# Performance work log

Hardware: AMD Instinct MI355X
Metric: run time of the kernel (lower is better)

The kernel has to match this reference:

```python
import jax, jax.numpy as jnp
import numpy as np

N = 100000
E = 3200000
IN_F = 256
OUT_F = 64
ALPHA = 0.2  # LeakyReLU negative slope


def setup_inputs() -> dict:
    key = jax.random.key(0)
    k1, k2, k3, k4 = jax.random.split(key, 4)
    adj = jax.random.randint(k1, (2, E), 0, N, dtype=jnp.int64)
    x = jax.random.normal(k2, (N, IN_F), dtype=jnp.float32)
    # xavier-normal-ish scales
    W_fc = jax.random.normal(k3, (OUT_F, IN_F), dtype=jnp.float32) * (1.414 * np.sqrt(2.0 / (IN_F + OUT_F)))
    b_fc = jnp.zeros((OUT_F,), dtype=jnp.float32)
    a = jax.random.normal(k4, (1, 2 * OUT_F), dtype=jnp.float32) * (1.414 * np.sqrt(2.0 / (1 + 2 * OUT_F)))
    return {"adj": adj, "x": x, "W_fc": W_fc, "b_fc": b_fc, "a": a}


def reference(adj, x, W_fc, b_fc, a):
    src = adj[0]  # [E]
    dst = adj[1]  # [E]
    h = x @ W_fc.T + b_fc                       # [N, OUT_F]
    a1, a2 = a[0, :OUT_F], a[0, OUT_F:]         # split of attention vector
    # e = leakyrelu(a . [h_src || h_dst]) computed without materializing concat
    s1 = h @ a1                                  # [N]
    s2 = h @ a2                                  # [N]
    e = s1[src] + s2[dst]                        # [E]
    e = jnp.where(e > 0, e, ALPHA * e)           # LeakyReLU
    # dgl edge_softmax: softmax over edges grouped by destination node
    m = jax.ops.segment_max(e, dst, num_segments=N)     # [N]
    ex = jnp.exp(e - m[dst])                             # [E]
    denom = jax.ops.segment_sum(ex, dst, num_segments=N) # [N]
    att = ex / denom[dst]                                # [E]
    # SparseTensor(row=src, col=dst, value=att) @ h -> out[src] += att * h[dst]
    h_prime = jax.ops.segment_sum(att[:, None] * h[dst], src, num_segments=N)  # [N, OUT_F]
    return jax.nn.elu(h_prime)  # concat=True branch
```

## Files before the change

kernel.cpp:

```cpp
#include <hip/hip_runtime.h>
#include <math.h>

#define N_NODES 100000
#define N_EDGES 3200000
#define IN_F 256
#define OUT_F 64
#define LRELU_ALPHA 0.2f
#define NBKT 782
#define CAP 4480

typedef unsigned short u16;
typedef __attribute__((ext_vector_type(8))) short short8;
typedef __attribute__((ext_vector_type(4))) float floatx4;

__device__ inline u16 f2bf(float f) {
  unsigned u = __float_as_uint(f);
  u += 0x7FFFu + ((u >> 16) & 1u);
  return (u16)(u >> 16);
}
__device__ inline float bf2f(u16 h) {
  return __uint_as_float(((unsigned)h) << 16);
}

__global__ __launch_bounds__(256) void k_prep(const float* __restrict__ W,
                                              u16* __restrict__ Wbf,
                                              int* __restrict__ sfill,
                                              int* __restrict__ dfill) {
  if (blockIdx.x < 64) {
    int i = blockIdx.x * 256 + threadIdx.x;
    Wbf[i] = f2bf(W[i]);
  } else {
    for (int i = threadIdx.x; i < NBKT; i += 256) {
      sfill[i] = 0;
      dfill[i] = 0;
    }
  }
}

__global__ __launch_bounds__(256) void k_linear(
    const float* __restrict__ x, const u16* __restrict__ Wbf,
    const float* __restrict__ b, const float* __restrict__ a,
    u16* __restrict__ hbf, float* __restrict__ s1, float* __restrict__ s2) {
  __shared__ u16 Wlds[64 * 264];

  const int t = threadIdx.x;
#pragma unroll
  for (int p = 0; p < 8; p++) {
    int c = p * 256 + t;
    int row = c >> 5;
    int kc = (c & 31) * 8;
    *(short8*)&Wlds[row * 264 + kc] = *(const short8*)&Wbf[row * 256 + kc];
  }
  __syncthreads();

  const int w = t >> 6;
  const int lane = t & 63;
  const int col = lane & 15;
  const int q = lane >> 4;
  const int m0 = blockIdx.x * 64 + w * 16;

  floatx4 acc[4];
#pragma unroll
  for (int nt = 0; nt < 4; nt++) acc[nt] = (floatx4){0.f, 0.f, 0.f, 0.f};

  int mrow = m0 + col;
  if (mrow > N_NODES - 1) mrow = N_NODES - 1;
  const float* xrow = x + (size_t)mrow * IN_F + q * 8;

#pragma unroll
  for (int kk = 0; kk < 8; kk++) {
    float4 f0 = *(const float4*)(xrow + kk * 32);
    float4 f1 = *(const float4*)(xrow + kk * 32 + 4);
    short8 af;
    af[0] = (short)f2bf(f0.x);
    af[1] = (short)f2bf(f0.y);
    af[2] = (short)f2bf(f0.z);
    af[3] = (short)f2bf(f0.w);
    af[4] = (short)f2bf(f1.x);
    af[5] = (short)f2bf(f1.y);
    af[6] = (short)f2bf(f1.z);
    af[7] = (short)f2bf(f1.w);
#pragma unroll
    for (int nt = 0; nt < 4; nt++) {
      short8 bfr = *(const short8*)&Wlds[(nt * 16 + col) * 264 + kk * 32 + q * 8];
      acc[nt] = __builtin_amdgcn_mfma_f32_16x16x32_bf16(af, bfr, acc[nt], 0, 0, 0);
    }
  }

  float bv[4], a1v[4], a2v[4];
#pragma unroll
  for (int nt = 0; nt < 4; nt++) {
    bv[nt] = b[nt * 16 + col];
    a1v[nt] = a[nt * 16 + col];
    a2v[nt] = a[OUT_F + nt * 16 + col];
  }
#pragma unroll
  for (int r = 0; r < 4; r++) {
    int node = m0 + q * 4 + r;
    float p1 = 0.f, p2 = 0.f;
#pragma unroll
    for (int nt = 0; nt < 4; nt++) {
      float hv = acc[nt][r] + bv[nt];
      if (node < N_NODES) hbf[(size_t)node * OUT_F + nt * 16 + col] = f2bf(hv);
      p1 = fmaf(hv, a1v[nt], p1);
      p2 = fmaf(hv, a2v[nt], p2);
    }
#pragma unroll
    for (int s = 1; s < 16; s <<= 1) {
      p1 += __shfl_xor(p1, s, 16);
      p2 += __shfl_xor(p2, s, 16);
    }
    if (col == 0 && node < N_NODES) {
      s1[node] = p1;
      s2[node] = p2;
    }
  }
}

#define EPT_P 8
__global__ __launch_bounds__(1024) void k_place(
    const int* __restrict__ src, const int* __restrict__ dst,
    const float* __restrict__ s1, const float* __restrict__ s2,
    int* __restrict__ sfill, int* __restrict__ dfill,
    float2* __restrict__ pairS, float2* __restrict__ pairD) {
  __shared__ int lcS[NBKT];
  __shared__ int lcD[NBKT];
  __shared__ int lbS[NBKT];
  __shared__ int lbD[NBKT];
  const int t = threadIdx.x;
  for (int i = t; i < NBKT; i += 1024) {
    lcS[i] = 0;
    lcD[i] = 0;
  }
  __syncthreads();

  int base = blockIdx.x * (1024 * EPT_P) + t;
  float ex[EPT_P];
  int pk[EPT_P];
  int bs[EPT_P];
#pragma unroll
  for (int j = 0; j < EPT_P; j++) {
    int e = base + j * 1024;
    if (e < N_EDGES) {
      int s = src[e];
      int d = dst[e];
      float v = s1[s] + s2[d];
      v = v > 0.f ? v : LRELU_ALPHA * v;
      ex[j] = __expf(v);
      pk[j] = d | ((s & 127) << 17);
      bs[j] = s >> 7;
      atomicAdd(&lcS[bs[j]], 1);
      atomicAdd(&lcD[d >> 7], 1);
    }
  }
  __syncthreads();
  for (int i = t; i < NBKT; i += 1024) {
    int c = lcS[i];
    if (c) lbS[i] = atomicAdd(&sfill[i], c);
    int c2 = lcD[i];
    if (c2) lbD[i] = atomicAdd(&dfill[i], c2);
  }
  __syncthreads();
  for (int i = t; i < NBKT; i += 1024) {
    lcS[i] = 0;
    lcD[i] = 0;
  }
  __syncthreads();
#pragma unroll
  for (int j = 0; j < EPT_P; j++) {
    int e = base + j * 1024;
    if (e < N_EDGES) {
      int d = pk[j] & 0x1FFFF;
      int r = atomicAdd(&lcS[bs[j]], 1);
      pairS[(size_t)bs[j] * CAP + lbS[bs[j]] + r] =
          make_float2(ex[j], __int_as_float(pk[j]));
      int bd = d >> 7;
      int r2 = atomicAdd(&lcD[bd], 1);
      pairD[(size_t)bd * CAP + lbD[bd] + r2] =
          make_float2(ex[j], __int_as_float(d & 127));
    }
  }
}

__global__ __launch_bounds__(256) void k_denom(const int* __restrict__ dfill,
                                               const float2* __restrict__ pairD,
                                               float* __restrict__ denom_r) {
  __shared__ float lacc[128];
  const int t = threadIdx.x;
  const int bkt = blockIdx.x;
  if (t < 128) lacc[t] = 0.f;
  __syncthreads();
  int beg = bkt * CAP;
  int end = beg + dfill[bkt];
  for (int i = beg + t; i < end; i += 256) {
    float2 p = pairD[i];
    atomicAdd(&lacc[__float_as_int(p.y)], p.x);
  }
  __syncthreads();
  if (t < 128) {
    int node = bkt * 128 + t;
    if (node < N_NODES) denom_r[node] = 1.0f / lacc[t];
  }
}

__global__ __launch_bounds__(256) void k_sort2(
    const int* __restrict__ sfill, const float2* __restrict__ pairS,
    const float* __restrict__ denom_r, float2* __restrict__ pairA,
    int2* __restrict__ rowbe) {
  __shared__ int lcnt[128];
  __shared__ int cursor[128];
  __shared__ int w0tot;
  const int t = threadIdx.x;
  const int bkt = blockIdx.x;
  if (t < 128) lcnt[t] = 0;
  __syncthreads();

  const int beg = bkt * CAP;
  const int end = beg + sfill[bkt];

  for (int i = beg + t; i < end; i += 256) {
    int pkv = __float_as_int(pairS[i].y);
    atomicAdd(&lcnt[(pkv >> 17) & 127], 1);
  }
  __syncthreads();

  const int lane = t & 63;
  int v = (t < 128) ? lcnt[t] : 0;
  int val = v;
#pragma unroll
  for (int ofs = 1; ofs < 64; ofs <<= 1) {
    int u = __shfl_up(val, ofs, 64);
    if (lane >= ofs) val += u;
  }
  if (t == 63) w0tot = val;
  __syncthreads();
  int excl = val - v + ((t >= 64 && t < 128) ? w0tot : 0);
  if (t < 128) {
    cursor[t] = beg + excl;
    int node = bkt * 128 + t;
    if (node < N_NODES) rowbe[node] = make_int2(beg + excl, beg + excl + v);
  }
  __syncthreads();

  for (int i = beg + t; i < end; i += 256) {
    float2 p = pairS[i];
    int pkv = __float_as_int(p.y);
    int sl = (pkv >> 17) & 127;
    int d = pkv & 0x1FFFF;
    float att = p.x * denom_r[d];
    int pos = atomicAdd(&cursor[sl], 1);
    pairA[pos] = make_float2(att, __int_as_float(d));
  }
}

__global__ __launch_bounds__(256) void k_aggregate(
    const int2* __restrict__ rowbe, const float2* __restrict__ pairA,
    const u16* __restrict__ hbf, float* __restrict__ out) {
  int wid = (blockIdx.x * 256 + threadIdx.x) >> 6;
  int lane = threadIdx.x & 63;
  int g = lane >> 4;
  int sl = lane & 15;
  int node = wid * 4 + g;
  int2 be = (node < N_NODES) ? rowbe[node] : make_int2(0, 0);
  float4 acc = make_float4(0.f, 0.f, 0.f, 0.f);
  int i = be.x;
  const int end = be.y;
  for (; i + 1 < end; i += 2) {
    float2 p0 = pairA[i];
    float2 p1 = pairA[i + 1];
    int d0 = __float_as_int(p0.y);
    int d1 = __float_as_int(p1.y);
    ushort4 q0 = *(const ushort4*)&hbf[(size_t)d0 * OUT_F + sl * 4];
    ushort4 q1 = *(const ushort4*)&hbf[(size_t)d1 * OUT_F + sl * 4];
    acc.x = fmaf(p0.x, bf2f(q0.x), acc.x);
    acc.y = fmaf(p0.x, bf2f(q0.y), acc.y);
    acc.z = fmaf(p0.x, bf2f(q0.z), acc.z);
    acc.w = fmaf(p0.x, bf2f(q0.w), acc.w);
    acc.x = fmaf(p1.x, bf2f(q1.x), acc.x);
    acc.y = fmaf(p1.x, bf2f(q1.y), acc.y);
    acc.z = fmaf(p1.x, bf2f(q1.z), acc.z);
    acc.w = fmaf(p1.x, bf2f(q1.w), acc.w);
  }
  if (i < end) {
    float2 p = pairA[i];
    int d = __float_as_int(p.y);
    ushort4 q = *(const ushort4*)&hbf[(size_t)d * OUT_F + sl * 4];
    acc.x = fmaf(p.x, bf2f(q.x), acc.x);
    acc.y = fmaf(p.x, bf2f(q.y), acc.y);
    acc.z = fmaf(p.x, bf2f(q.z), acc.z);
    acc.w = fmaf(p.x, bf2f(q.w), acc.w);
  }
  if (node < N_NODES) {
    float4 o;
    o.x = acc.x > 0.f ? acc.x : expm1f(acc.x);
    o.y = acc.y > 0.f ? acc.y : expm1f(acc.y);
    o.z = acc.z > 0.f ? acc.z : expm1f(acc.z);
    o.w = acc.w > 0.f ? acc.w : expm1f(acc.w);
    *(float4*)(out + (size_t)node * OUT_F + sl * 4) = o;
  }
}

extern "C" void kernel_launch(void* const* d_in, const int* in_sizes, int n_in,
                              void* d_out, int out_size, void* d_ws,
                              size_t ws_size, hipStream_t stream) {
  const int* adj = (const int*)d_in[0];
  const float* x = (const float*)d_in[1];
  const float* W = (const float*)d_in[2];
  const float* b = (const float*)d_in[3];
  const float* a = (const float*)d_in[4];
  float* out = (float*)d_out;

  float* ws = (float*)d_ws;
  float* s1v = ws;
  float* s2v = ws + 100000;
  float* denom_r = ws + 200000;
  int* sfill = (int*)(ws + 300000);
  int* dfill = (int*)(ws + 300800);
  int2* rowbe = (int2*)(ws + 301600);
  float2* pairS = (float2*)(ws + 501600);
  float2* pairD = (float2*)(ws + 7508320);
  u16* hbf = (u16*)(ws + 14515040);
  u16* Wbf = (u16*)(ws + 17715040);

  float2* pairA = pairD;

  const int* src = adj;
  const int* dst = adj + N_EDGES;

  k_prep<<<65, 256, 0, stream>>>(W, Wbf, sfill, dfill);
  k_linear<<<(N_NODES + 63) / 64, 256, 0, stream>>>(x, Wbf, b, a, hbf, s1v, s2v);
  k_place<<<(N_EDGES + 1024 * EPT_P - 1) / (1024 * EPT_P), 1024, 0, stream>>>(
      src, dst, s1v, s2v, sfill, dfill, pairS, pairD);
  k_denom<<<NBKT, 256, 0, stream>>>(dfill, pairD, denom_r);
  k_sort2<<<NBKT, 256, 0, stream>>>(sfill, pairS, denom_r, pairA, rowbe);
  k_aggregate<<<(N_NODES + 15) / 16, 256, 0, stream>>>(rowbe, pairA, hbf, out);
}
```

Before: 421.2 us.

## Replace destination bucketing and denom kernel with global atomic denominator accumulation

Stops scattering edges into destination buckets (pairD) and drops the separate k_denom pass. Softmax denominators are now accumulated with global float atomicAdd per edge inside k_place, and k_sort2 takes the reciprocal with a fast rcp. The prep kernel zeroes sfill plus the denom array in one contiguous region. This removes a 25.6MB scatter write, its re-read and a kernel launch, at the cost of 3.2M contended global float atomics.

Measured after the change: 496.2 us. +17.8%, slower.

```diff
diff --git a/kernel.cpp b/kernel.cpp
--- a/kernel.cpp
+++ b/kernel.cpp
@@ -22,17 +22,17 @@
   return __uint_as_float(((unsigned)h) << 16);
 }
 
+#define ZERO_WORDS (800 + 100000)
 __global__ __launch_bounds__(256) void k_prep(const float* __restrict__ W,
                                               u16* __restrict__ Wbf,
-                                              int* __restrict__ sfill,
-                                              int* __restrict__ dfill) {
+                                              int* __restrict__ zbase) {
   if (blockIdx.x < 64) {
     int i = blockIdx.x * 256 + threadIdx.x;
     Wbf[i] = f2bf(W[i]);
   } else {
-    for (int i = threadIdx.x; i < NBKT; i += 256) {
-      sfill[i] = 0;
-      dfill[i] = 0;
+    int i4 = (blockIdx.x - 64) * 256 + threadIdx.x;
+    if (i4 < ZERO_WORDS / 4) {
+      ((int4*)zbase)[i4] = make_int4(0, 0, 0, 0);
     }
   }
 }
@@ -121,17 +121,12 @@
 __global__ __launch_bounds__(1024) void k_place(
     const int* __restrict__ src, const int* __restrict__ dst,
     const float* __restrict__ s1, const float* __restrict__ s2,
-    int* __restrict__ sfill, int* __restrict__ dfill,
-    float2* __restrict__ pairS, float2* __restrict__ pairD) {
+    int* __restrict__ sfill, float* __restrict__ denom,
+    float2* __restrict__ pairS) {
   __shared__ int lcS[NBKT];
-  __shared__ int lcD[NBKT];
   __shared__ int lbS[NBKT];
-  __shared__ int lbD[NBKT];
   const int t = threadIdx.x;
-  for (int i = t; i < NBKT; i += 1024) {
-    lcS[i] = 0;
-    lcD[i] = 0;
-  }
+  for (int i = t; i < NBKT; i += 1024) lcS[i] = 0;
   __syncthreads();
 
   int base = blockIdx.x * (1024 * EPT_P) + t;
@@ -150,62 +145,32 @@
       pk[j] = d | ((s & 127) << 17);
       bs[j] = s >> 7;
       atomicAdd(&lcS[bs[j]], 1);
-      atomicAdd(&lcD[d >> 7], 1);
     }
   }
   __syncthreads();
   for (int i = t; i < NBKT; i += 1024) {
     int c = lcS[i];
     if (c) lbS[i] = atomicAdd(&sfill[i], c);
-    int c2 = lcD[i];
-    if (c2) lbD[i] = atomicAdd(&dfill[i], c2);
-  }
-  __syncthreads();
-  for (int i = t; i < NBKT; i += 1024) {
-    lcS[i] = 0;
-    lcD[i] = 0;
-  }
+  }
+  __syncthreads();
+  for (int i = t; i < NBKT; i += 1024) lcS[i] = 0;
   __syncthreads();
 #pragma unroll
   for (int j = 0; j < EPT_P; j++) {
     int e = base + j * 1024;
     if (e < N_EDGES) {
       int d = pk[j] & 0x1FFFF;
+      atomicAdd(&denom[d], ex[j]);
       int r = atomicAdd(&lcS[bs[j]], 1);
       pairS[(size_t)bs[j] * CAP + lbS[bs[j]] + r] =
           make_float2(ex[j], __int_as_float(pk[j]));
-      int bd = d >> 7;
-      int r2 = atomicAdd(&lcD[bd], 1);
-      pairD[(size_t)bd * CAP + lbD[bd] + r2] =
-          make_float2(ex[j], __int_as_float(d & 127));
-    }
-  }
-}
-
-__global__ __launch_bounds__(256) void k_denom(const int* __restrict__ dfill,
-                                               const float2* __restrict__ pairD,
-                                               float* __restrict__ denom_r) {
-  __shared__ float lacc[128];
-  const int t = threadIdx.x;
-  const int bkt = blockIdx.x;
-  if (t < 128) lacc[t] = 0.f;
-  __syncthreads();
-  int beg = bkt * CAP;
-  int end = beg + dfill[bkt];
-  for (int i = beg + t; i < end; i += 256) {
-    float2 p = pairD[i];
-    atomicAdd(&lacc[__float_as_int(p.y)], p.x);
-  }
-  __syncthreads();
-  if (t < 128) {
-    int node = bkt * 128 + t;
-    if (node < N_NODES) denom_r[node] = 1.0f / lacc[t];
+    }
   }
 }
 
 __global__ __launch_bounds__(256) void k_sort2(
     const int* __restrict__ sfill, const float2* __restrict__ pairS,
-    const float* __restrict__ denom_r, float2* __restrict__ pairA,
+    const float* __restrict__ denom, float2* __restrict__ pairA,
     int2* __restrict__ rowbe) {
   __shared__ int lcnt[128];
   __shared__ int cursor[128];
@@ -247,7 +212,7 @@
     int pkv = __float_as_int(p.y);
     int sl = (pkv >> 17) & 127;
     int d = pkv & 0x1FFFF;
-    float att = p.x * denom_r[d];
+    float att = p.x * __builtin_amdgcn_rcpf(denom[d]);
     int pos = atomicAdd(&cursor[sl], 1);
     pairA[pos] = make_float2(att, __int_as_float(d));
   }
@@ -313,25 +278,21 @@
   float* ws = (float*)d_ws;
   float* s1v = ws;
   float* s2v = ws + 100000;
-  float* denom_r = ws + 200000;
-  int* sfill = (int*)(ws + 300000);
-  int* dfill = (int*)(ws + 300800);
-  int2* rowbe = (int2*)(ws + 301600);
-  float2* pairS = (float2*)(ws + 501600);
-  float2* pairD = (float2*)(ws + 7508320);
-  u16* hbf = (u16*)(ws + 14515040);
-  u16* Wbf = (u16*)(ws + 17715040);
-
-  float2* pairA = pairD;
+  int* sfill = (int*)(ws + 200000);
+  float* denom = ws + 200800;
+  int2* rowbe = (int2*)(ws + 300800);
+  float2* pairS = (float2*)(ws + 500800);
+  float2* pairA = (float2*)(ws + 7507520);
+  u16* hbf = (u16*)(ws + 14514240);
+  u16* Wbf = (u16*)(ws + 17714240);
 
   const int* src = adj;
   const int* dst = adj + N_EDGES;
 
-  k_prep<<<65, 256, 0, stream>>>(W, Wbf, sfill, dfill);
+  k_prep<<<164, 256, 0, stream>>>(W, Wbf, sfill);
   k_linear<<<(N_NODES + 63) / 64, 256, 0, stream>>>(x, Wbf, b, a, hbf, s1v, s2v);
   k_place<<<(N_EDGES + 1024 * EPT_P - 1) / (1024 * EPT_P), 1024, 0, stream>>>(
-      src, dst, s1v, s2v, sfill, dfill, pairS, pairD);
-  k_denom<<<NBKT, 256, 0, stream>>>(dfill, pairD, denom_r);
-  k_sort2<<<NBKT, 256, 0, stream>>>(sfill, pairS, denom_r, pairA, rowbe);
+      src, dst, s1v, s2v, sfill, denom, pairS);
+  k_sort2<<<NBKT, 256, 0, stream>>>(sfill, pairS, denom, pairA, rowbe);
   k_aggregate<<<(N_NODES + 15) / 16, 256, 0, stream>>>(rowbe, pairA, hbf, out);
 }
```

## Stage bucketed edge pairs in LDS for coalesced scatter in placement kernel

Applied to the files above, without the earlier changes.

The placement kernel now groups each block's edges by bucket in shared memory before writing them to global memory. Each bucket's run becomes a contiguous, mostly coalesced write, where before every edge was an independent random 8-byte store. The source and destination passes run one after the other and reuse the same staging buffer. Block size drops from 1024 to 512 threads so the roughly 40 KB staging buffer fits, at the cost of more barriers and a second counting pass.

New measurement: 409.9 us. 1.03x faster.

```diff
diff --git a/kernel.cpp b/kernel.cpp
--- a/kernel.cpp
+++ b/kernel.cpp
@@ -117,30 +117,35 @@
   }
 }
 
+#define PBT 512
 #define EPT_P 8
-__global__ __launch_bounds__(1024) void k_place(
+#define PEB (PBT * EPT_P)
+__global__ __launch_bounds__(PBT) void k_place(
     const int* __restrict__ src, const int* __restrict__ dst,
     const float* __restrict__ s1, const float* __restrict__ s2,
     int* __restrict__ sfill, int* __restrict__ dfill,
     float2* __restrict__ pairS, float2* __restrict__ pairD) {
-  __shared__ int lcS[NBKT];
-  __shared__ int lcD[NBKT];
-  __shared__ int lbS[NBKT];
-  __shared__ int lbD[NBKT];
+  __shared__ int lc[NBKT];
+  __shared__ int ofs[NBKT];
+  __shared__ int gbase[NBKT];
+  __shared__ int tot;
+  __shared__ float2 stage[PEB];
+  __shared__ u16 stageB[PEB];
+
   const int t = threadIdx.x;
-  for (int i = t; i < NBKT; i += 1024) {
-    lcS[i] = 0;
-    lcD[i] = 0;
-  }
-  __syncthreads();
-
-  int base = blockIdx.x * (1024 * EPT_P) + t;
+  const int base = blockIdx.x * PEB + t;
+
   float ex[EPT_P];
   int pk[EPT_P];
   int bs[EPT_P];
+
+  for (int i = t; i < NBKT; i += PBT) lc[i] = 0;
+  if (t == 0) tot = 0;
+  __syncthreads();
+
 #pragma unroll
   for (int j = 0; j < EPT_P; j++) {
-    int e = base + j * 1024;
+    int e = base + j * PBT;
     if (e < N_EDGES) {
       int s = src[e];
       int d = dst[e];
@@ -149,36 +154,81 @@
       ex[j] = __expf(v);
       pk[j] = d | ((s & 127) << 17);
       bs[j] = s >> 7;
-      atomicAdd(&lcS[bs[j]], 1);
-      atomicAdd(&lcD[d >> 7], 1);
-    }
-  }
-  __syncthreads();
-  for (int i = t; i < NBKT; i += 1024) {
-    int c = lcS[i];
-    if (c) lbS[i] = atomicAdd(&sfill[i], c);
-    int c2 = lcD[i];
-    if (c2) lbD[i] = atomicAdd(&dfill[i], c2);
-  }
-  __syncthreads();
-  for (int i = t; i < NBKT; i += 1024) {
-    lcS[i] = 0;
-    lcD[i] = 0;
-  }
-  __syncthreads();
+      atomicAdd(&lc[bs[j]], 1);
+    } else {
+      bs[j] = -1;
+    }
+  }
+  __syncthreads();
+
+  for (int i = t; i < NBKT; i += PBT) {
+    int c = lc[i];
+    if (c) {
+      gbase[i] = i * CAP + atomicAdd(&sfill[i], c);
+      ofs[i] = atomicAdd(&tot, c);
+    }
+  }
+  __syncthreads();
+  const int nval = tot;
+  for (int i = t; i < NBKT; i += PBT) lc[i] = 0;
+  __syncthreads();
+
 #pragma unroll
   for (int j = 0; j < EPT_P; j++) {
-    int e = base + j * 1024;
-    if (e < N_EDGES) {
+    if (bs[j] >= 0) {
+      int r = atomicAdd(&lc[bs[j]], 1);
+      int idx = ofs[bs[j]] + r;
+      stage[idx] = make_float2(ex[j], __int_as_float(pk[j]));
+      stageB[idx] = (u16)bs[j];
+    }
+  }
+  __syncthreads();
+
+  for (int i = t; i < nval; i += PBT) {
+    int bkt = stageB[i];
+    pairS[gbase[bkt] + (i - ofs[bkt])] = stage[i];
+  }
+  __syncthreads();
+
+  for (int i = t; i < NBKT; i += PBT) lc[i] = 0;
+  if (t == 0) tot = 0;
+  __syncthreads();
+#pragma unroll
+  for (int j = 0; j < EPT_P; j++) {
+    if (bs[j] >= 0) {
+      int bd = (pk[j] & 0x1FFFF) >> 7;
+      atomicAdd(&lc[bd], 1);
+    }
+  }
+  __syncthreads();
+
+  for (int i = t; i < NBKT; i += PBT) {
+    int c = lc[i];
+    if (c) {
+      gbase[i] = i * CAP + atomicAdd(&dfill[i], c);
+      ofs[i] = atomicAdd(&tot, c);
+    }
+  }
+  __syncthreads();
+  for (int i = t; i < NBKT; i += PBT) lc[i] = 0;
+  __syncthreads();
+
+#pragma unroll
+  for (int j = 0; j < EPT_P; j++) {
+    if (bs[j] >= 0) {
       int d = pk[j] & 0x1FFFF;
-      int r = atomicAdd(&lcS[bs[j]], 1);
-      pairS[(size_t)bs[j] * CAP + lbS[bs[j]] + r] =
-          make_float2(ex[j], __int_as_float(pk[j]));
       int bd = d >> 7;
-      int r2 = atomicAdd(&lcD[bd], 1);
-      pairD[(size_t)bd * CAP + lbD[bd] + r2] =
-          make_float2(ex[j], __int_as_float(d & 127));
-    }
+      int r = atomicAdd(&lc[bd], 1);
+      int idx = ofs[bd] + r;
+      stage[idx] = make_float2(ex[j], __int_as_float(d & 127));
+      stageB[idx] = (u16)bd;
+    }
+  }
+  __syncthreads();
+
+  for (int i = t; i < nval; i += PBT) {
+    int bkt = stageB[i];
+    pairD[gbase[bkt] + (i - ofs[bkt])] = stage[i];
   }
 }
 
@@ -329,7 +379,7 @@
 
   k_prep<<<65, 256, 0, stream>>>(W, Wbf, sfill, dfill);
   k_linear<<<(N_NODES + 63) / 64, 256, 0, stream>>>(x, Wbf, b, a, hbf, s1v, s2v);
-  k_place<<<(N_EDGES + 1024 * EPT_P - 1) / (1024 * EPT_P), 1024, 0, stream>>>(
+  k_place<<<(N_EDGES + PEB - 1) / PEB, PBT, 0, stream>>>(
       src, dst, s1v, s2v, sfill, dfill, pairS, pairD);
   k_denom<<<NBKT, 256, 0, stream>>>(dfill, pairD, denom_r);
   k_sort2<<<NBKT, 256, 0, stream>>>(sfill, pairS, denom_r, pairA, rowbe);
```
